# Performance work log

Measured on AMD Instinct MI355X. Metric: run time of the kernel, lower is better.

## Reference

```python
import jax, jax.numpy as jnp
import numpy as np

L, B, D_IN = 2048, 32, 1024
DENSE, HID = 256, 128
NUM_CLASSES = 2
NT = NUM_CLASSES + 2  # + START, STOP tags
START, STOP = NT - 2, NT - 1
IMPOSSIBLE = -1e4


def setup_inputs() -> dict:
    key = jax.random.key(0)
    ks = jax.random.split(key, 14)
    s = 0.05
    src = jax.random.uniform(ks[0], (L, B, D_IN), dtype=jnp.float32)
    fc1_w = jax.random.normal(ks[1], (DENSE, D_IN), jnp.float32) * s
    fc1_b = jax.random.normal(ks[2], (DENSE,), jnp.float32) * s
    w_ih_f = jax.random.normal(ks[3], (4 * HID, DENSE), jnp.float32) * s
    w_hh_f = jax.random.normal(ks[4], (4 * HID, HID), jnp.float32) * s
    b_ih_f = jax.random.normal(ks[5], (4 * HID,), jnp.float32) * s
    b_hh_f = jax.random.normal(ks[6], (4 * HID,), jnp.float32) * s
    w_ih_b = jax.random.normal(ks[7], (4 * HID, DENSE), jnp.float32) * s
    w_hh_b = jax.random.normal(ks[8], (4 * HID, HID), jnp.float32) * s
    b_ih_b = jax.random.normal(ks[9], (4 * HID,), jnp.float32) * s
    b_hh_b = jax.random.normal(ks[10], (4 * HID,), jnp.float32) * s
    crf_w = jax.random.normal(ks[11], (NT, 2 * HID), jnp.float32) * s
    crf_b = jax.random.normal(ks[12], (NT,), jnp.float32) * s
    transitions = jax.random.normal(ks[13], (NT, NT), jnp.float32)
    transitions = transitions.at[START, :].set(IMPOSSIBLE)  # no transition TO start
    transitions = transitions.at[:, STOP].set(IMPOSSIBLE)   # no transition FROM stop
    return dict(src=src, fc1_w=fc1_w, fc1_b=fc1_b,
                w_ih_f=w_ih_f, w_hh_f=w_hh_f, b_ih_f=b_ih_f, b_hh_f=b_hh_f,
                w_ih_b=w_ih_b, w_hh_b=w_hh_b, b_ih_b=b_ih_b, b_hh_b=b_hh_b,
                crf_w=crf_w, crf_b=crf_b, transitions=transitions)


def _lstm_dir(x, w_ih, w_hh, b_ih, b_hh):
    # x: [L, B, D]; PyTorch gate order i, f, g, o
    pre = jnp.einsum('lbd,hd->lbh', x, w_ih) + b_ih + b_hh  # [L, B, 4H]
    h_dim = w_hh.shape[1]
    bsz = x.shape[1]

    def step(carry, p):
        h, c = carry
        g = p + h @ w_hh.T
        i, f, gg, o = jnp.split(g, 4, axis=-1)
        c = jax.nn.sigmoid(f) * c + jax.nn.sigmoid(i) * jnp.tanh(gg)
        h = jax.nn.sigmoid(o) * jnp.tanh(c)
        return (h, c), h

    init = (jnp.zeros((bsz, h_dim), x.dtype), jnp.zeros((bsz, h_dim), x.dtype))
    _, hs = jax.lax.scan(step, init, pre)
    return hs  # [L, B, H]


def reference(src, fc1_w, fc1_b, w_ih_f, w_hh_f, b_ih_f, b_hh_f,
              w_ih_b, w_hh_b, b_ih_b, b_hh_b, crf_w, crf_b, transitions):
    masks = (jnp.sum(src, axis=2) > 0).T.astype(src.dtype)  # [B, L]
    x = jax.nn.relu(jnp.einsum('lbd,od->lbo', src, fc1_w) + fc1_b)  # [L,B,DENSE]
    hf = _lstm_dir(x, w_ih_f, w_hh_f, b_ih_f, b_hh_f)
    hb = _lstm_dir(x[::-1], w_ih_b, w_hh_b, b_ih_b, b_hh_b)[::-1]
    feats = jnp.concatenate([hf, hb], axis=-1)  # [L, B, 2H] (dropout = eval identity)
    emit = jnp.einsum('lbh,ch->lbc', feats, crf_w) + crf_b  # [L, B, NT]

    bsz = src.shape[1]
    init_score = jnp.full((bsz, NT), IMPOSSIBLE, emit.dtype).at[:, START].set(0.0)

    def vstep(max_score, inp):
        e_t, m_t = inp  # [B, NT], [B]
        acc = max_score[:, None, :] + transitions[None]  # [B, to, from]
        bp = jnp.argmax(acc, axis=-1)                    # [B, NT]
        new = jnp.max(acc, axis=-1) + e_t
        m = m_t[:, None]
        return new * m + max_score * (1.0 - m), bp

    final, bps = jax.lax.scan(vstep, init_score, (emit, masks.T))  # bps: [L, B, NT]
    final = final + transitions[STOP]
    best_score = jnp.max(final, axis=-1)   # [B]
    best_tag = jnp.argmax(final, axis=-1)  # [B]

    def bstep(tag, bp_t):
        prev = jnp.take_along_axis(bp_t, tag[:, None], axis=1)[:, 0]
        return prev, prev

    _, prevs = jax.lax.scan(bstep, best_tag, bps[1:], reverse=True)  # tags t=0..L-2
    tags = jnp.concatenate([prevs, best_tag[None]], axis=0).T  # [B, L]
    return best_score, tags
```

## Files before the change

### kernel.cpp

```cpp
#include <hip/hip_runtime.h>
#include <hip/hip_bf16.h>
#include <stdint.h>

#define L_SEQ 2048
#define BATCH 32
#define D_IN 1024
#define DENSE 256
#define HID 128
#define GATES 512
#define NT 4
#define START_TAG 2
#define STOP_TAG 3
#define IMPOSSIBLE -10000.0f

template<bool RELU, bool DUAL>
__global__ __launch_bounds__(256)
void gemm_nt(const float* __restrict__ A, const float* __restrict__ Bw,
             const float* __restrict__ b1, const float* __restrict__ b2,
             float* __restrict__ C, int M, int N, int K)
{
    __shared__ __align__(16) float As[2][16][132];
    __shared__ __align__(16) float Bs[2][16][132];

    const int tid = threadIdx.x;
    const int tx = tid & 15;
    const int ty = tid >> 4;
    const int m0 = blockIdx.x * 128;
    const int n0 = blockIdx.y * 128;

    const int lrow = tid >> 2;
    const int lcol = (tid & 3) * 4;

    const float* aptr = &A[(size_t)(m0 + lrow) * K + lcol];
    const float* bptr = &Bw[(size_t)(n0 + lrow) * K + lcol];
    const size_t rstride = (size_t)64 * K;

    float acc[8][8];
#pragma unroll
    for (int i = 0; i < 8; ++i)
#pragma unroll
        for (int j = 0; j < 8; ++j) acc[i][j] = 0.f;

    {
        float4 a0 = *(const float4*)(aptr);
        float4 a1 = *(const float4*)(aptr + rstride);
        float4 v0 = *(const float4*)(bptr);
        float4 v1 = *(const float4*)(bptr + rstride);
        As[0][lcol + 0][lrow] = a0.x; As[0][lcol + 1][lrow] = a0.y;
        As[0][lcol + 2][lrow] = a0.z; As[0][lcol + 3][lrow] = a0.w;
        As[0][lcol + 0][lrow + 64] = a1.x; As[0][lcol + 1][lrow + 64] = a1.y;
        As[0][lcol + 2][lrow + 64] = a1.z; As[0][lcol + 3][lrow + 64] = a1.w;
        Bs[0][lcol + 0][lrow] = v0.x; Bs[0][lcol + 1][lrow] = v0.y;
        Bs[0][lcol + 2][lrow] = v0.z; Bs[0][lcol + 3][lrow] = v0.w;
        Bs[0][lcol + 0][lrow + 64] = v1.x; Bs[0][lcol + 1][lrow + 64] = v1.y;
        Bs[0][lcol + 2][lrow + 64] = v1.z; Bs[0][lcol + 3][lrow + 64] = v1.w;
    }
    __syncthreads();

    int buf = 0;
    for (int k0 = 0; k0 < K; k0 += 16) {
        const int kn = (k0 + 16 < K) ? (k0 + 16) : k0;
        float4 na0 = *(const float4*)(aptr + kn);
        float4 na1 = *(const float4*)(aptr + kn + rstride);
        float4 nb0 = *(const float4*)(bptr + kn);
        float4 nb1 = *(const float4*)(bptr + kn + rstride);

#pragma unroll
        for (int kk = 0; kk < 16; ++kk) {
            float4 av0 = *(const float4*)&As[buf][kk][ty * 8];
            float4 av1 = *(const float4*)&As[buf][kk][ty * 8 + 4];
            float4 bv0 = *(const float4*)&Bs[buf][kk][tx * 8];
            float4 bv1 = *(const float4*)&Bs[buf][kk][tx * 8 + 4];
            float a[8], b[8];
            a[0] = av0.x; a[1] = av0.y; a[2] = av0.z; a[3] = av0.w;
            a[4] = av1.x; a[5] = av1.y; a[6] = av1.z; a[7] = av1.w;
            b[0] = bv0.x; b[1] = bv0.y; b[2] = bv0.z; b[3] = bv0.w;
            b[4] = bv1.x; b[5] = bv1.y; b[6] = bv1.z; b[7] = bv1.w;
#pragma unroll
            for (int i = 0; i < 8; ++i)
#pragma unroll
                for (int j = 0; j < 8; ++j)
                    acc[i][j] = fmaf(a[i], b[j], acc[i][j]);
        }

        const int nb = buf ^ 1;
        As[nb][lcol + 0][lrow] = na0.x; As[nb][lcol + 1][lrow] = na0.y;
        As[nb][lcol + 2][lrow] = na0.z; As[nb][lcol + 3][lrow] = na0.w;
        As[nb][lcol + 0][lrow + 64] = na1.x; As[nb][lcol + 1][lrow + 64] = na1.y;
        As[nb][lcol + 2][lrow + 64] = na1.z; As[nb][lcol + 3][lrow + 64] = na1.w;
        Bs[nb][lcol + 0][lrow] = nb0.x; Bs[nb][lcol + 1][lrow] = nb0.y;
        Bs[nb][lcol + 2][lrow] = nb0.z; Bs[nb][lcol + 3][lrow] = nb0.w;
        Bs[nb][lcol + 0][lrow + 64] = nb1.x; Bs[nb][lcol + 1][lrow + 64] = nb1.y;
        Bs[nb][lcol + 2][lrow + 64] = nb1.z; Bs[nb][lcol + 3][lrow + 64] = nb1.w;

        __syncthreads();
        buf = nb;
    }

    float bia[8];
#pragma unroll
    for (int j = 0; j < 8; ++j) {
        int col = n0 + tx * 8 + j;
        bia[j] = b1[col] + (DUAL ? b2[col] : 0.f);
    }
#pragma unroll
    for (int r = 0; r < 8; ++r) {
        int row = m0 + ty * 8 + r;
        float v[8];
#pragma unroll
        for (int j = 0; j < 8; ++j) {
            v[j] = acc[r][j] + bia[j];
            if (RELU) v[j] = fmaxf(v[j], 0.f);
        }
        float* cp = &C[(size_t)row * N + n0 + tx * 8];
        *(float4*)&cp[0] = make_float4(v[0], v[1], v[2], v[3]);
        *(float4*)&cp[4] = make_float4(v[4], v[5], v[6], v[7]);
    }
}

__device__ __forceinline__ float sigf(float x) { return 1.f / (1.f + expf(-x)); }

__global__ __launch_bounds__(512, 2)
void lstm_kernel(const float* __restrict__ preF, const float* __restrict__ preB,
                 const float* __restrict__ wF, const float* __restrict__ wB,
                 float* __restrict__ hF, float* __restrict__ hB)
{
    const int g = blockIdx.x;
    const int dir = g >> 5;
    const int b = g & 31;
    const float* pre = dir ? preB : preF;
    const float* W   = dir ? wB : wF;
    float* hout      = dir ? hB : hF;

    const int t = threadIdx.x;

    float w[128];
#pragma unroll
    for (int k = 0; k < 128; k += 4) {
        float4 wv = *(const float4*)&W[(size_t)t * 128 + k];
        w[k + 0] = wv.x; w[k + 1] = wv.y; w[k + 2] = wv.z; w[k + 3] = wv.w;
    }

    __shared__ __align__(16) float h_s[128];
    __shared__ __align__(16) float g_s[512];

    float c_reg = 0.f;
    if (t < 128) h_s[t] = 0.f;
    __syncthreads();

    const float* prow = pre + ((size_t)(dir ? (L_SEQ - 1) : 0) * BATCH + b) * GATES + t;
    const intptr_t pstep = (dir ? -(intptr_t)1 : (intptr_t)1) * (intptr_t)(BATCH * GATES);

    float pre_next = *prow;

    for (int step = 0; step < L_SEQ; ++step) {
        const int tt = dir ? (L_SEQ - 1 - step) : step;
        float pre_cur = pre_next;
        if (step + 1 < L_SEQ) prow += pstep;
        pre_next = *prow;

        float a0 = pre_cur, a1 = 0.f, a2 = 0.f, a3 = 0.f;
#pragma unroll
        for (int k = 0; k < 128; k += 4) {
            float4 hv = *(const float4*)&h_s[k];
            a0 = fmaf(w[k + 0], hv.x, a0);
            a1 = fmaf(w[k + 1], hv.y, a1);
            a2 = fmaf(w[k + 2], hv.z, a2);
            a3 = fmaf(w[k + 3], hv.w, a3);
        }
        g_s[t] = (a0 + a1) + (a2 + a3);

        asm volatile("s_waitcnt lgkmcnt(0)\n\ts_barrier" ::: "memory");

        float h_keep = 0.f;
        if (t < 128) {
            float iv = g_s[t];
            float fv = g_s[t + 128];
            float gv = g_s[t + 256];
            float ov = g_s[t + 384];
            c_reg = sigf(fv) * c_reg + sigf(iv) * tanhf(gv);
            h_keep = sigf(ov) * tanhf(c_reg);
            h_s[t] = h_keep;
        }

        asm volatile("s_waitcnt lgkmcnt(0)\n\ts_barrier" ::: "memory");

        if (t < 128)
            hout[((size_t)tt * BATCH + b) * HID + t] = h_keep;
    }
}

__global__ __launch_bounds__(256)
void emit_kernel(const float* __restrict__ hf, const float* __restrict__ hb,
                 const float* __restrict__ crf_w, const float* __restrict__ crf_b,
                 float* __restrict__ emit)
{
    const int idx = blockIdx.x * 256 + threadIdx.x;
    const int r = idx >> 2;
    const int c = idx & 3;
    const float* wf = &crf_w[c * 256];
    float acc = crf_b[c];
#pragma unroll 4
    for (int k = 0; k < 128; k += 4) {
        float4 hv = *(const float4*)&hf[(size_t)r * 128 + k];
        float4 wv = *(const float4*)&wf[k];
        acc = fmaf(hv.x, wv.x, acc); acc = fmaf(hv.y, wv.y, acc);
        acc = fmaf(hv.z, wv.z, acc); acc = fmaf(hv.w, wv.w, acc);
    }
#pragma unroll 4
    for (int k = 0; k < 128; k += 4) {
        float4 hv = *(const float4*)&hb[(size_t)r * 128 + k];
        float4 wv = *(const float4*)&wf[128 + k];
        acc = fmaf(hv.x, wv.x, acc); acc = fmaf(hv.y, wv.y, acc);
        acc = fmaf(hv.z, wv.z, acc); acc = fmaf(hv.w, wv.w, acc);
    }
    emit[idx] = acc;
}

__global__ __launch_bounds__(64)
void viterbi_kernel(const float* __restrict__ emit, const float* __restrict__ trans,
                    float* __restrict__ out)
{
    const int lane = threadIdx.x;
    const int b_loc = lane >> 2;
    const int i = lane & 3;
    const int b = blockIdx.x * 16 + b_loc;
    const int base = lane & ~3;

    __shared__ uint8_t bp_s[L_SEQ * 16];
    __shared__ uint8_t tag_s[L_SEQ * 16];

    float T0 = trans[i * 4 + 0];
    float T1 = trans[i * 4 + 1];
    float T2 = trans[i * 4 + 2];
    float T3 = trans[i * 4 + 3];
    float tstop = trans[STOP_TAG * 4 + i];

    float s = (i == START_TAG) ? 0.f : IMPOSSIBLE;

    float e_cur = emit[(size_t)0 * BATCH * NT + b * NT + i];
    for (int t = 0; t < L_SEQ; ++t) {
        float e_next = 0.f;
        if (t + 1 < L_SEQ)
            e_next = emit[(size_t)(t + 1) * BATCH * NT + b * NT + i];

        float s0 = __shfl(s, base + 0, 64);
        float s1 = __shfl(s, base + 1, 64);
        float s2 = __shfl(s, base + 2, 64);
        float s3 = __shfl(s, base + 3, 64);

        float a0 = s0 + T0, a1 = s1 + T1, a2 = s2 + T2, a3 = s3 + T3;
        float best = a0; int arg = 0;
        if (a1 > best) { best = a1; arg = 1; }
        if (a2 > best) { best = a2; arg = 2; }
        if (a3 > best) { best = a3; arg = 3; }

        s = best + e_cur;
        e_cur = e_next;

        int A0 = __shfl(arg, base + 0, 64);
        int A1 = __shfl(arg, base + 1, 64);
        int A2 = __shfl(arg, base + 2, 64);
        int A3 = __shfl(arg, base + 3, 64);
        if (i == 0)
            bp_s[t * 16 + b_loc] = (uint8_t)(A0 | (A1 << 2) | (A2 << 4) | (A3 << 6));
    }

    float f = s + tstop;
    float f0 = __shfl(f, base + 0, 64);
    float f1 = __shfl(f, base + 1, 64);
    float f2 = __shfl(f, base + 2, 64);
    float f3 = __shfl(f, base + 3, 64);
    float best = f0; int btag = 0;
    if (f1 > best) { best = f1; btag = 1; }
    if (f2 > best) { best = f2; btag = 2; }
    if (f3 > best) { best = f3; btag = 3; }

    if (i == 0) {
        out[b] = best;
        int tag = btag;
        tag_s[(L_SEQ - 1) * 16 + b_loc] = (uint8_t)tag;
        for (int t = L_SEQ - 1; t >= 1; --t) {
            uint8_t byte = bp_s[t * 16 + b_loc];
            tag = (byte >> (2 * tag)) & 3;
            tag_s[(t - 1) * 16 + b_loc] = (uint8_t)tag;
        }
    }
    __syncthreads();

    float* tout = out + BATCH;
    for (int bb = 0; bb < 16; ++bb) {
        int bg = blockIdx.x * 16 + bb;
        for (int t0 = lane; t0 < L_SEQ; t0 += 64)
            tout[(size_t)bg * L_SEQ + t0] = (float)tag_s[t0 * 16 + bb];
    }
}

extern "C" void kernel_launch(void* const* d_in, const int* in_sizes, int n_in,
                              void* d_out, int out_size, void* d_ws, size_t ws_size,
                              hipStream_t stream)
{
    const float* src    = (const float*)d_in[0];
    const float* fc1_w  = (const float*)d_in[1];
    const float* fc1_b  = (const float*)d_in[2];
    const float* w_ih_f = (const float*)d_in[3];
    const float* w_hh_f = (const float*)d_in[4];
    const float* b_ih_f = (const float*)d_in[5];
    const float* b_hh_f = (const float*)d_in[6];
    const float* w_ih_b = (const float*)d_in[7];
    const float* w_hh_b = (const float*)d_in[8];
    const float* b_ih_b = (const float*)d_in[9];
    const float* b_hh_b = (const float*)d_in[10];
    const float* crf_w  = (const float*)d_in[11];
    const float* crf_b  = (const float*)d_in[12];
    const float* trans  = (const float*)d_in[13];

    char* ws = (char*)d_ws;
    const size_t MB = 1024 * 1024;
    float* x    = (float*)(ws);
    float* preF = (float*)(ws + 64 * MB);
    float* preB = (float*)(ws + 192 * MB);
    float* hf   = (float*)(ws);
    float* hb   = (float*)(ws + 32 * MB);
    float* emit = (float*)(ws + 64 * MB);

    const int M = L_SEQ * BATCH;

    {
        dim3 grid(M / 128, DENSE / 128);
        gemm_nt<true, false><<<grid, 256, 0, stream>>>(src, fc1_w, fc1_b, nullptr,
                                                       x, M, DENSE, D_IN);
    }
    {
        dim3 grid(M / 128, GATES / 128);
        gemm_nt<false, true><<<grid, 256, 0, stream>>>(x, w_ih_f, b_ih_f, b_hh_f,
                                                       preF, M, GATES, DENSE);
        gemm_nt<false, true><<<grid, 256, 0, stream>>>(x, w_ih_b, b_ih_b, b_hh_b,
                                                       preB, M, GATES, DENSE);
    }
    lstm_kernel<<<64, 512, 0, stream>>>(preF, preB, w_hh_f, w_hh_b, hf, hb);

    emit_kernel<<<(M * NT) / 256, 256, 0, stream>>>(hf, hb, crf_w, crf_b, emit);

    viterbi_kernel<<<2, 64, 0, stream>>>(emit, trans, (float*)d_out);
}
```

Before: 4.799 ms.

## Restructure LSTM recurrence with two gate rows per thread and lane broadcasts

Each LSTM block now uses 256 threads, and each thread computes two gate rows with the weights held in registers. Even/odd thread pairs exchange gates through a shuffle, so the gate shared-memory staging and one barrier per step go away. The hidden state is double-buffered in shared memory and broadcast with readlane, and the output store moves before the barrier. The cost is doubled register pressure (256 weight floats per thread) and a serial chain of readlane operations per step.

```diff
diff --git a/kernel.cpp b/kernel.cpp
--- a/kernel.cpp
+++ b/kernel.cpp
@@ -120,7 +120,11 @@
 
 __device__ __forceinline__ float sigf(float x) { return 1.f / (1.f + expf(-x)); }
 
-__global__ __launch_bounds__(512, 2)
+__device__ __forceinline__ float bcast(float v, int lane) {
+    return __int_as_float(__builtin_amdgcn_readlane(__float_as_int(v), lane));
+}
+
+__global__ __launch_bounds__(256, 1)
 void lstm_kernel(const float* __restrict__ preF, const float* __restrict__ preB,
                  const float* __restrict__ wF, const float* __restrict__ wB,
                  float* __restrict__ hF, float* __restrict__ hB)
@@ -133,60 +137,67 @@
     float* hout      = dir ? hB : hF;
 
     const int t = threadIdx.x;
-
-    float w[128];
+    const int lane = t & 63;
+    const int j = t >> 1;
+    const int odd = t & 1;
+    const int r0 = j + odd * 128;
+    const int r1 = r0 + 256;
+
+    float w0[128], w1[128];
 #pragma unroll
     for (int k = 0; k < 128; k += 4) {
-        float4 wv = *(const float4*)&W[(size_t)t * 128 + k];
-        w[k + 0] = wv.x; w[k + 1] = wv.y; w[k + 2] = wv.z; w[k + 3] = wv.w;
-    }
-
-    __shared__ __align__(16) float h_s[128];
-    __shared__ __align__(16) float g_s[512];
+        float4 wv = *(const float4*)&W[(size_t)r0 * 128 + k];
+        w0[k + 0] = wv.x; w0[k + 1] = wv.y; w0[k + 2] = wv.z; w0[k + 3] = wv.w;
+        float4 wu = *(const float4*)&W[(size_t)r1 * 128 + k];
+        w1[k + 0] = wu.x; w1[k + 1] = wu.y; w1[k + 2] = wu.z; w1[k + 3] = wu.w;
+    }
+
+    __shared__ __align__(16) float h_s[2][128];
 
     float c_reg = 0.f;
-    if (t < 128) h_s[t] = 0.f;
+    if (t < 128) { h_s[0][t] = 0.f; h_s[1][t] = 0.f; }
     __syncthreads();
 
-    const float* prow = pre + ((size_t)(dir ? (L_SEQ - 1) : 0) * BATCH + b) * GATES + t;
+    const float* prow = pre + ((size_t)(dir ? (L_SEQ - 1) : 0) * BATCH + b) * GATES;
     const intptr_t pstep = (dir ? -(intptr_t)1 : (intptr_t)1) * (intptr_t)(BATCH * GATES);
 
-    float pre_next = *prow;
-
+    float pre0 = prow[r0];
+    float pre1 = prow[r1];
+
+    int buf = 0;
     for (int step = 0; step < L_SEQ; ++step) {
         const int tt = dir ? (L_SEQ - 1 - step) : step;
-        float pre_cur = pre_next;
+        float p0 = pre0, p1 = pre1;
         if (step + 1 < L_SEQ) prow += pstep;
-        pre_next = *prow;
-
-        float a0 = pre_cur, a1 = 0.f, a2 = 0.f, a3 = 0.f;
-#pragma unroll
-        for (int k = 0; k < 128; k += 4) {
-            float4 hv = *(const float4*)&h_s[k];
-            a0 = fmaf(w[k + 0], hv.x, a0);
-            a1 = fmaf(w[k + 1], hv.y, a1);
-            a2 = fmaf(w[k + 2], hv.z, a2);
-            a3 = fmaf(w[k + 3], hv.w, a3);
-        }
-        g_s[t] = (a0 + a1) + (a2 + a3);
+        pre0 = prow[r0];
+        pre1 = prow[r1];
+
+        float hreg0 = h_s[buf][lane];
+        float hreg1 = h_s[buf][lane + 64];
+
+        float a00 = p0, a01 = 0.f, a10 = p1, a11 = 0.f;
+#pragma unroll
+        for (int k = 0; k < 128; ++k) {
+            const float src = (k < 64) ? hreg0 : hreg1;
+            float hk = bcast(src, k & 63);
+            if (k < 64) { a00 = fmaf(w0[k], hk, a00); a10 = fmaf(w1[k], hk, a10); }
+            else        { a01 = fmaf(w0[k], hk, a01); a11 = fmaf(w1[k], hk, a11); }
+        }
+        float G0 = a00 + a01;
+        float G1 = a10 + a11;
+
+        float fv = __shfl_xor(G0, 1, 64);
+        float ov = __shfl_xor(G1, 1, 64);
+
+        if (!odd) {
+            c_reg = sigf(fv) * c_reg + sigf(G0) * tanhf(G1);
+            float h_keep = sigf(ov) * tanhf(c_reg);
+            h_s[buf ^ 1][j] = h_keep;
+            hout[((size_t)tt * BATCH + b) * HID + j] = h_keep;
+        }
 
         asm volatile("s_waitcnt lgkmcnt(0)\n\ts_barrier" ::: "memory");
-
-        float h_keep = 0.f;
-        if (t < 128) {
-            float iv = g_s[t];
-            float fv = g_s[t + 128];
-            float gv = g_s[t + 256];
-            float ov = g_s[t + 384];
-            c_reg = sigf(fv) * c_reg + sigf(iv) * tanhf(gv);
-            h_keep = sigf(ov) * tanhf(c_reg);
-            h_s[t] = h_keep;
-        }
-
-        asm volatile("s_waitcnt lgkmcnt(0)\n\ts_barrier" ::: "memory");
-
-        if (t < 128)
-            hout[((size_t)tt * BATCH + b) * HID + t] = h_keep;
+        buf ^= 1;
     }
 }
 
@@ -338,7 +349,7 @@
         gemm_nt<false, true><<<grid, 256, 0, stream>>>(x, w_ih_b, b_ih_b, b_hh_b,
                                                        preB, M, GATES, DENSE);
     }
-    lstm_kernel<<<64, 512, 0, stream>>>(preF, preB, w_hh_f, w_hh_b, hf, hb);
+    lstm_kernel<<<64, 256, 0, stream>>>(preF, preB, w_hh_f, w_hh_b, hf, hb);
 
     emit_kernel<<<(M * NT) / 256, 256, 0, stream>>>(hf, hb, crf_w, crf_b, emit);
 
```

New measurement: 5.089 ms. +6.0%, slower.
